# Optimization experiments

Measured on AMD Instinct MI355X. Metric: run time of the kernel, lower is better.

The kernel has to match this reference:

```python
import jax, jax.numpy as jnp
import numpy as np

N = 50000        # graph_size / n_nodes
E = 1250000      # n_edges
NFEAT = 128
NHID = 64
NCLASS = 47
NLAYERS = 4
DT = 1.0
ALPHA = 1.0


def setup_inputs() -> dict:
    key = jax.random.key(0)
    ks = jax.random.split(key, 12)
    stdv = 1.0 / np.sqrt(NHID)  # reset_params uses uniform(-1/sqrt(nhid), 1/sqrt(nhid))
    u = lambda k, shp: jax.random.uniform(k, shp, jnp.float32, -stdv, stdv)
    return {
        "x": jax.random.normal(ks[0], (N, NFEAT), jnp.float32),
        "edge_index": jax.random.randint(ks[1], (2, E), 0, N, jnp.int32),
        # Linear weights stored as (in, out); torch computes x @ W.T + b, same math.
        "enc_w": u(ks[2], (NFEAT, NHID)),
        "enc_b": u(ks[3], (NHID,)),
        "conv_w": u(ks[4], (NHID, NHID)),   # GCNConv.lin weight (no bias)
        "conv_b": u(ks[5], (NHID,)),        # GCNConv bias (added after aggregation)
        "res_w": u(ks[6], (NHID, NHID)),
        "res_b": u(ks[7], (NHID,)),
        "dec_w": u(ks[8], (NHID, NCLASS)),
        "dec_b": u(ks[9], (NCLASS,)),
        # original inits epsilons to zeros; small noise makes the gate nontrivial
        "epsilons": 0.01 * jax.random.normal(ks[10], (NLAYERS, NHID), jnp.float32),
    }


def reference(x, edge_index, enc_w, enc_b, conv_w, conv_b, res_w, res_b,
              dec_w, dec_b, epsilons):
    n = x.shape[0]
    loop = jnp.arange(n, dtype=edge_index.dtype)
    row = jnp.concatenate([edge_index[0], loop])  # add self-loops (PyG default)
    col = jnp.concatenate([edge_index[1], loop])
    deg = jax.ops.segment_sum(jnp.ones_like(row, x.dtype), col, num_segments=n)
    dinv = jnp.where(deg > 0, jax.lax.rsqrt(deg), 0.0)
    norm = dinv[row] * dinv[col]  # D^{-1/2} (A+I) D^{-1/2}

    # eval mode: dropout is identity
    X = jax.nn.relu(x @ enc_w + enc_b)
    X0 = X
    for i in range(NLAYERS):
        h = X @ conv_w  # conv.lin(X), shared by conv and residual v1
        conv_out = jax.ops.segment_sum(h[row] * norm[:, None], col,
                                       num_segments=n) + conv_b
        res = -(h @ res_w + res_b)          # res_connection_v1
        coeff = 1.0 + jnp.tanh(epsilons[i])[None, :]  # (1, nhid) broadcast over nodes
        X0 = X0 * coeff + DT * (jax.nn.relu(conv_out + res) - ALPHA * X)
        X = X0
    return X @ dec_w + dec_b
```

## Files before the change

### kernel.cpp

```cpp
#include <hip/hip_runtime.h>
#include <hip/hip_bf16.h>
#include <math.h>

#define NFEAT 128
#define NHID 64
#define NCLASS 47
#define NLAYERS 4
#define CAP 80
#define NBUCK 8
#define BSHIFT 13
#define BCAP 262144
#define BK_EPB 4096
#define FILL2_KB 64
#define AFW 72

typedef __attribute__((ext_vector_type(8))) _Float16 half8;
typedef __attribute__((ext_vector_type(4))) float f32x4;


__global__ __launch_bounds__(256) void k_init(int* __restrict__ deg,
                                              int* __restrict__ gcur,
                                              const float* __restrict__ conv_w,
                                              const float* __restrict__ res_w,
                                              const float* __restrict__ conv_b,
                                              const float* __restrict__ res_b,
                                              const float* __restrict__ eps,
                                              const float* __restrict__ dec_w,
                                              _Float16* __restrict__ Whb,
                                              _Float16* __restrict__ W2hb,
                                              _Float16* __restrict__ Dechb,
                                              float* __restrict__ bc,
                                              float* __restrict__ te,
                                              int n, int nzero) {
    int gid = blockIdx.x * 256 + threadIdx.x;
    if (gid < nzero) {
        if (gid < n) deg[gid] = 0;
        return;
    }
    int t = gid - nzero;
    if (t < 512) {
        int jt = t >> 7, kt = (t >> 6) & 1, l = t & 63;
        int j = jt * 16 + (l & 15);
        int kb = kt * 32 + (l >> 4) * 8;
#pragma unroll
        for (int i = 0; i < 8; ++i)
            Whb[t * 8 + i] = (_Float16)conv_w[(kb + i) * 64 + j];
        return;
    }
    t -= 512;
    if (t < 512) {
        int jt = t >> 7, kt = (t >> 6) & 1, l = t & 63;
        int j = jt * 16 + (l & 15);
        int kb = kt * 32 + (l >> 4) * 8;
#pragma unroll
        for (int i = 0; i < 8; ++i) {
            int k = kb + i;
            float acc = 0.0f;
#pragma unroll 8
            for (int o = 0; o < 64; ++o)
                acc = fmaf(conv_w[k * 64 + o], res_w[o * 64 + j], acc);
            W2hb[t * 8 + i] = (_Float16)acc;
        }
        return;
    }
    t -= 512;
    if (t < 512) {
        int jt = t >> 7, kt = (t >> 6) & 1, l = t & 63;
        int j = jt * 16 + (l & 15);
        int kb = kt * 32 + (l >> 4) * 8;
#pragma unroll
        for (int i = 0; i < 8; ++i) {
            int k = kb + i;
            Dechb[t * 8 + i] = (j < NCLASS) ? (_Float16)dec_w[k * NCLASS + j]
                                            : (_Float16)0.0f;
        }
        return;
    }
    t -= 512;
    if (t < NLAYERS * NHID) {
        te[t] = tanhf(eps[t]);
        if (t < NHID) bc[t] = conv_b[t] - res_b[t];
        if (t < NBUCK) gcur[t] = 0;
    }
}


__global__ __launch_bounds__(256) void k_bucket(const int* __restrict__ row,
                                                const int* __restrict__ col,
                                                int* __restrict__ gcur,
                                                unsigned int* __restrict__ buckets,
                                                int e) {
    __shared__ int lc[BK_EPB];
    __shared__ int lr[BK_EPB];
    __shared__ int cnt[NBUCK], basep[NBUCK], cnt2[NBUCK];
    const int tid = threadIdx.x;
    const int start = blockIdx.x * BK_EPB;
    const int m = min(BK_EPB, e - start);
    if (tid < NBUCK) { cnt[tid] = 0; cnt2[tid] = 0; }
    __syncthreads();
    for (int i = tid; i < m; i += 256) {
        int c = col[start + i];
        int r = row[start + i];
        lc[i] = c; lr[i] = r;
        atomicAdd(&cnt[c >> BSHIFT], 1);
    }
    __syncthreads();
    if (tid < NBUCK) basep[tid] = atomicAdd(&gcur[tid], cnt[tid]);
    __syncthreads();
    for (int i = tid; i < m; i += 256) {
        int c = lc[i], r = lr[i];
        int s = c >> BSHIFT;
        int dst = basep[s] + atomicAdd(&cnt2[s], 1);
        if (dst < BCAP)
            buckets[(size_t)s * BCAP + dst] = ((unsigned)r << 16) | (unsigned)c;
    }
}


__global__ __launch_bounds__(256) void k_fill2(const unsigned int* __restrict__ buckets,
                                               const int* __restrict__ gcur,
                                               int* __restrict__ deg,
                                               unsigned short* __restrict__ csr) {
    const int s = blockIdx.x & (NBUCK - 1);
    const int k = blockIdx.x >> 3;
    const int cnt = min(gcur[s], BCAP);
    const int per = (cnt + FILL2_KB - 1) / FILL2_KB;
    const int lo = k * per;
    const int hi = min(lo + per, cnt);
    const unsigned int* bp = buckets + (size_t)s * BCAP;
    for (int i = lo + (int)threadIdx.x; i < hi; i += 256) {
        unsigned int v = bp[i];
        int c = (int)(v & 0xffffu);
        int r = (int)(v >> 16);
        int pos = atomicAdd(&deg[c], 1);
        if (pos < CAP) csr[(size_t)c * CAP + pos] = (unsigned short)r;
    }
}


__global__ void k_dinv(const int* __restrict__ deg, float* __restrict__ dinv,
                       float* __restrict__ rsq, unsigned short* __restrict__ csr,
                       _Float16* __restrict__ Y0, _Float16* __restrict__ Y1, int n) {
    int i = blockIdx.x * blockDim.x + threadIdx.x;
    if (i < n) {
        int d = deg[i];
        if (d > CAP) d = CAP;
        float d1 = (float)(deg[i] + 1);
        dinv[i] = rsqrtf(d1);
        rsq[i] = sqrtf(d1);
        int end = (d + 7) & ~7;
        if (end > CAP) end = CAP;
        for (int s = d; s < end; ++s)
            csr[(size_t)i * CAP + s] = (unsigned short)n;
    }
    if (i < NHID) {
        Y0[(size_t)n * NHID + i] = (_Float16)0.0f;
        Y1[(size_t)n * NHID + i] = (_Float16)0.0f;
    }
}


__global__ __launch_bounds__(256) void k_encoder(const float* __restrict__ x,
                                                 const float* __restrict__ w,
                                                 const float* __restrict__ b,
                                                 const float* __restrict__ dinv,
                                                 _Float16* __restrict__ Y, int n) {
    __shared__ float xs[16][NFEAT];
    const int wid = threadIdx.x >> 6;
    const int j = threadIdx.x & 63;
    const int base = blockIdx.x * 16 + wid * 4;
    for (int m = 0; m < 4; ++m) {
        int node = base + m;
        float a = 0.f, c = 0.f;
        if (node < n) {
            a = x[node * NFEAT + j];
            c = x[node * NFEAT + 64 + j];
        }
        xs[wid * 4 + m][j] = a;
        xs[wid * 4 + m][j + 64] = c;
    }
    float acc[4] = {0.f, 0.f, 0.f, 0.f};
#pragma unroll 4
    for (int k4 = 0; k4 < NFEAT / 4; ++k4) {
        int k = k4 * 4;
        float w0 = w[(k + 0) * 64 + j];
        float w1 = w[(k + 1) * 64 + j];
        float w2 = w[(k + 2) * 64 + j];
        float w3 = w[(k + 3) * 64 + j];
        for (int m = 0; m < 4; ++m) {
            const float4 xv = *reinterpret_cast<const float4*>(&xs[wid * 4 + m][k]);
            acc[m] = fmaf(xv.x, w0, fmaf(xv.y, w1, fmaf(xv.z, w2, fmaf(xv.w, w3, acc[m]))));
        }
    }
    float bj = b[j];
    for (int m = 0; m < 4; ++m) {
        int node = base + m;
        if (node < n) {
            float v = fmaxf(acc[m] + bj, 0.0f);
            Y[node * NHID + j] = (_Float16)(v * dinv[node]);
        }
    }
}


__global__ __launch_bounds__(256, 4) void k_layer(
    const half8* __restrict__ Y8c, _Float16* __restrict__ Ynext,
    const int* __restrict__ deg, const unsigned short* __restrict__ csr,
    const float* __restrict__ dinv, const float* __restrict__ rsq,
    const half8* __restrict__ Whb, const half8* __restrict__ W2hb,
    const half8* __restrict__ Dechb,
    const float* __restrict__ bc, const float* __restrict__ te,
    const float* __restrict__ dec_b, float* __restrict__ out, int n, int last) {
    __shared__ _Float16 Af[16][AFW];
    __shared__ _Float16 Xf[16][AFW];
    const int wid = threadIdx.x >> 6;
    const int lane = threadIdx.x & 63;
    const int g = lane >> 4;
    const int l = lane & 15;
    const int c = l & 7;
    const unsigned sh = (l & 8) << 1;
    const int base = blockIdx.x * 16 + wid * 4;
    const int mynode = base + g;
    const bool gact = mynode < n;
    const int gn = gact ? mynode : 0;
    const int rown = gact ? mynode : n;
    const float dcg = dinv[gn];
    const float rcg = rsq[gn];
    int d = gact ? deg[gn] : 0;
    if (d > CAP) d = CAP;
    const int nit = (d + 7) >> 3;

    float acc[8] = {0.f, 0.f, 0.f, 0.f, 0.f, 0.f, 0.f, 0.f};
    const uint4* cp = reinterpret_cast<const uint4*>(csr + (size_t)gn * CAP);

    uint4 rA = cp[0];
    int a0 = (int)((rA.x >> sh) & 0xffffu);
    int a1 = (int)((rA.y >> sh) & 0xffffu);
    int a2 = (int)((rA.z >> sh) & 0xffffu);
    int a3 = (int)((rA.w >> sh) & 0xffffu);
    half8 A0 = Y8c[(size_t)(a0 * 8 + c)];
    half8 A1 = Y8c[(size_t)(a1 * 8 + c)];
    half8 A2 = Y8c[(size_t)(a2 * 8 + c)];
    half8 A3 = Y8c[(size_t)(a3 * 8 + c)];
    int it = 0;
    for (; it + 1 < nit; it += 2) {
        uint4 rB = cp[it + 1];
        int b0 = (int)((rB.x >> sh) & 0xffffu);
        int b1 = (int)((rB.y >> sh) & 0xffffu);
        int b2 = (int)((rB.z >> sh) & 0xffffu);
        int b3 = (int)((rB.w >> sh) & 0xffffu);
        half8 B0 = Y8c[(size_t)(b0 * 8 + c)];
        half8 B1 = Y8c[(size_t)(b1 * 8 + c)];
        half8 B2 = Y8c[(size_t)(b2 * 8 + c)];
        half8 B3 = Y8c[(size_t)(b3 * 8 + c)];
#pragma unroll
        for (int i = 0; i < 8; ++i)
            acc[i] += ((float)A0[i] + (float)A1[i]) + ((float)A2[i] + (float)A3[i]);
        rA = cp[it + 2];
        a0 = (int)((rA.x >> sh) & 0xffffu);
        a1 = (int)((rA.y >> sh) & 0xffffu);
        a2 = (int)((rA.z >> sh) & 0xffffu);
        a3 = (int)((rA.w >> sh) & 0xffffu);
        A0 = Y8c[(size_t)(a0 * 8 + c)];
        A1 = Y8c[(size_t)(a1 * 8 + c)];
        A2 = Y8c[(size_t)(a2 * 8 + c)];
        A3 = Y8c[(size_t)(a3 * 8 + c)];
#pragma unroll
        for (int i = 0; i < 8; ++i)
            acc[i] += ((float)B0[i] + (float)B1[i]) + ((float)B2[i] + (float)B3[i]);
    }
    if (it < nit) {
#pragma unroll
        for (int i = 0; i < 8; ++i)
            acc[i] += ((float)A0[i] + (float)A1[i]) + ((float)A2[i] + (float)A3[i]);
    }
#pragma unroll
    for (int i = 0; i < 8; ++i) acc[i] += __shfl_xor(acc[i], 8);

    if (l < 8) {
        half8 yc = Y8c[(size_t)(rown * 8 + c)];
        half8 hg, hx;
#pragma unroll
        for (int i = 0; i < 8; ++i) {
            float ycf = (float)yc[i];
            hg[i] = (_Float16)((acc[i] + ycf) * dcg);
            hx[i] = (_Float16)(ycf * rcg);
        }
        *reinterpret_cast<half8*>(&Af[wid * 4 + g][c * 8]) = hg;
        *reinterpret_cast<half8*>(&Xf[wid * 4 + g][c * 8]) = hx;
    }

    float dv[4];
#pragma unroll
    for (int i = 0; i < 4; ++i) dv[i] = __shfl(dcg, i * 16);

    const int ar = (wid * 4 + (lane & 15)) & 15;
    const int aq = (lane >> 4) * 8;
    half8 aG0 = *reinterpret_cast<const half8*>(&Af[ar][aq]);
    half8 aG1 = *reinterpret_cast<const half8*>(&Af[ar][32 + aq]);
    half8 aX0 = *reinterpret_cast<const half8*>(&Xf[ar][aq]);
    half8 aX1 = *reinterpret_cast<const half8*>(&Xf[ar][32 + aq]);
    const f32x4 zero = {0.f, 0.f, 0.f, 0.f};

#pragma unroll
    for (int jt = 0; jt < 4; ++jt) {
        half8 bG0 = Whb[(jt * 2 + 0) * 64 + lane];
        half8 bG1 = Whb[(jt * 2 + 1) * 64 + lane];
        half8 bX0 = W2hb[(jt * 2 + 0) * 64 + lane];
        half8 bX1 = W2hb[(jt * 2 + 1) * 64 + lane];
        f32x4 dG = __builtin_amdgcn_mfma_f32_16x16x32_f16(aG0, bG0, zero, 0, 0, 0);
        dG = __builtin_amdgcn_mfma_f32_16x16x32_f16(aG1, bG1, dG, 0, 0, 0);
        f32x4 dX = __builtin_amdgcn_mfma_f32_16x16x32_f16(aX0, bX0, zero, 0, 0, 0);
        dX = __builtin_amdgcn_mfma_f32_16x16x32_f16(aX1, bX1, dX, 0, 0, 0);
        if (lane < 16) {
            int j = jt * 16 + lane;
            float tej = te[j], bcj = bc[j];
#pragma unroll
            for (int i = 0; i < 4; ++i) {
                int node = base + i;
                float xf = (float)Xf[wid * 4 + i][j];
                float xn = xf * tej + fmaxf(dG[i] + bcj - dX[i], 0.0f);
                if (!last) {
                    if (node < n)
                        Ynext[(size_t)node * NHID + j] = (_Float16)(xn * dv[i]);
                } else {
                    Af[wid * 4 + i][j] = (_Float16)xn;
                }
            }
        }
    }

    if (last) {
        half8 aD0 = *reinterpret_cast<const half8*>(&Af[ar][aq]);
        half8 aD1 = *reinterpret_cast<const half8*>(&Af[ar][32 + aq]);
#pragma unroll
        for (int jt = 0; jt < 4; ++jt) {
            half8 bD0 = Dechb[(jt * 2 + 0) * 64 + lane];
            half8 bD1 = Dechb[(jt * 2 + 1) * 64 + lane];
            f32x4 dd = __builtin_amdgcn_mfma_f32_16x16x32_f16(aD0, bD0, zero, 0, 0, 0);
            dd = __builtin_amdgcn_mfma_f32_16x16x32_f16(aD1, bD1, dd, 0, 0, 0);
            if (lane < 16) {
                int j = jt * 16 + lane;
                if (j < NCLASS) {
                    float db = dec_b[j];
#pragma unroll
                    for (int i = 0; i < 4; ++i) {
                        int node = base + i;
                        if (node < n) out[(size_t)node * NCLASS + j] = dd[i] + db;
                    }
                }
            }
        }
    }
}

extern "C" void kernel_launch(void* const* d_in, const int* in_sizes, int n_in,
                              void* d_out, int out_size, void* d_ws, size_t ws_size,
                              hipStream_t stream) {
    const float* x      = (const float*)d_in[0];
    const int*   edges  = (const int*)d_in[1];
    const float* enc_w  = (const float*)d_in[2];
    const float* enc_b  = (const float*)d_in[3];
    const float* conv_w = (const float*)d_in[4];
    const float* conv_b = (const float*)d_in[5];
    const float* res_w  = (const float*)d_in[6];
    const float* res_b  = (const float*)d_in[7];
    const float* dec_w  = (const float*)d_in[8];
    const float* dec_b  = (const float*)d_in[9];
    const float* eps    = (const float*)d_in[10];
    float* out = (float*)d_out;

    const int n = in_sizes[0] / NFEAT;
    const int e = in_sizes[1] / 2;
    const int* row = edges;
    const int* col = edges + e;

    char* p = (char*)d_ws;
    unsigned short* csr = (unsigned short*)p;
    p += ((size_t)n * CAP * 2 + 64 + 15) & ~(size_t)15;
    unsigned int* buckets = (unsigned int*)p;  p += (size_t)NBUCK * BCAP * 4;
    _Float16* Y0 = (_Float16*)p;  p += (((size_t)(n + 1) * NHID * 2 + 15) & ~(size_t)15);
    _Float16* Y1 = (_Float16*)p;  p += (((size_t)(n + 1) * NHID * 2 + 15) & ~(size_t)15);
    int*   deg  = (int*)p;    p += (size_t)n * 4;
    float* dinv = (float*)p;  p += (size_t)n * 4;
    float* rsq  = (float*)p;  p += (size_t)n * 4;
    int*   gcur = (int*)p;    p += 64;
    float* bc   = (float*)p;  p += NHID * 4;
    float* te   = (float*)p;  p += NLAYERS * NHID * 4;
    _Float16* Whb   = (_Float16*)p;  p += 4096 * 2;
    _Float16* W2hb  = (_Float16*)p;  p += 4096 * 2;
    _Float16* Dechb = (_Float16*)p;  p += 4096 * 2;
    if ((size_t)(p - (char*)d_ws) > ws_size) return;

    const int nzero = ((n + 255) / 256) * 256;
    const int init_blocks = (nzero + 1792 + 255) / 256;

    k_init<<<init_blocks, 256, 0, stream>>>(deg, gcur, conv_w, res_w, conv_b, res_b,
                                            eps, dec_w, Whb, W2hb, Dechb, bc, te,
                                            n, nzero);
    const int bblocks = (e + BK_EPB - 1) / BK_EPB;
    k_bucket<<<bblocks, 256, 0, stream>>>(row, col, gcur, buckets, e);
    k_fill2<<<NBUCK * FILL2_KB, 256, 0, stream>>>(buckets, gcur, deg, csr);
    k_dinv<<<(n + 255) / 256, 256, 0, stream>>>(deg, dinv, rsq, csr, Y0, Y1, n);

    const int tblocks = (n + 15) / 16;
    k_encoder<<<tblocks, 256, 0, stream>>>(x, enc_w, enc_b, dinv, Y0, n);

    for (int l = 0; l < NLAYERS; ++l) {
        _Float16* ycur = (l & 1) ? Y1 : Y0;
        _Float16* ynxt = (l & 1) ? Y0 : Y1;
        k_layer<<<tblocks, 256, 0, stream>>>((const half8*)ycur, ynxt, deg, csr,
                                             dinv, rsq, (const half8*)Whb,
                                             (const half8*)W2hb, (const half8*)Dechb,
                                             bc, te + l * NHID, dec_b, out, n,
                                             (l == NLAYERS - 1) ? 1 : 0);
    }
}
```

Before: 257.6 us.

## Use fine-grained node buckets with shared-memory degree counters in CSR fill

Edges are now bucketed into 128 slices of 512 destination nodes instead of 8 large buckets. Each CSR-fill block owns one slice, counts degrees with shared-memory atomics, then writes the degree array once. This removes the global atomics on the degree array and the separate degree-zeroing pass in the init kernel. In exchange the fill kernel runs only one block per slice, which may leave the GPU under-occupied. Correctness also depends on no bucket exceeding the smaller per-bucket capacity.

```diff
diff --git a/kernel.cpp b/kernel.cpp
--- a/kernel.cpp
+++ b/kernel.cpp
@@ -7,19 +7,18 @@
 #define NCLASS 47
 #define NLAYERS 4
 #define CAP 80
-#define NBUCK 8
-#define BSHIFT 13
-#define BCAP 262144
+#define NBUCK 128
+#define BSHIFT 9
+#define BSLICE 512
+#define BCAP 16384
 #define BK_EPB 4096
-#define FILL2_KB 64
 #define AFW 72
 
 typedef __attribute__((ext_vector_type(8))) _Float16 half8;
 typedef __attribute__((ext_vector_type(4))) float f32x4;
 
 
-__global__ __launch_bounds__(256) void k_init(int* __restrict__ deg,
-                                              int* __restrict__ gcur,
+__global__ __launch_bounds__(256) void k_init(int* __restrict__ gcur,
                                               const float* __restrict__ conv_w,
                                               const float* __restrict__ res_w,
                                               const float* __restrict__ conv_b,
@@ -30,14 +29,8 @@
                                               _Float16* __restrict__ W2hb,
                                               _Float16* __restrict__ Dechb,
                                               float* __restrict__ bc,
-                                              float* __restrict__ te,
-                                              int n, int nzero) {
-    int gid = blockIdx.x * 256 + threadIdx.x;
-    if (gid < nzero) {
-        if (gid < n) deg[gid] = 0;
-        return;
-    }
-    int t = gid - nzero;
+                                              float* __restrict__ te) {
+    int t = blockIdx.x * 256 + threadIdx.x;
     if (t < 512) {
         int jt = t >> 7, kt = (t >> 6) & 1, l = t & 63;
         int j = jt * 16 + (l & 15);
@@ -96,7 +89,7 @@
     const int tid = threadIdx.x;
     const int start = blockIdx.x * BK_EPB;
     const int m = min(BK_EPB, e - start);
-    if (tid < NBUCK) { cnt[tid] = 0; cnt2[tid] = 0; }
+    for (int i = tid; i < NBUCK; i += 256) { cnt[i] = 0; cnt2[i] = 0; }
     __syncthreads();
     for (int i = tid; i < m; i += 256) {
         int c = col[start + i];
@@ -105,7 +98,8 @@
         atomicAdd(&cnt[c >> BSHIFT], 1);
     }
     __syncthreads();
-    if (tid < NBUCK) basep[tid] = atomicAdd(&gcur[tid], cnt[tid]);
+    for (int i = tid; i < NBUCK; i += 256)
+        if (cnt[i] > 0) basep[i] = atomicAdd(&gcur[i], cnt[i]);
     __syncthreads();
     for (int i = tid; i < m; i += 256) {
         int c = lc[i], r = lr[i];
@@ -120,21 +114,26 @@
 __global__ __launch_bounds__(256) void k_fill2(const unsigned int* __restrict__ buckets,
                                                const int* __restrict__ gcur,
                                                int* __restrict__ deg,
-                                               unsigned short* __restrict__ csr) {
-    const int s = blockIdx.x & (NBUCK - 1);
-    const int k = blockIdx.x >> 3;
+                                               unsigned short* __restrict__ csr,
+                                               int n) {
+    __shared__ int cur[BSLICE];
+    const int s = blockIdx.x;
+    const int tid = threadIdx.x;
+    for (int i = tid; i < BSLICE; i += 256) cur[i] = 0;
+    __syncthreads();
     const int cnt = min(gcur[s], BCAP);
-    const int per = (cnt + FILL2_KB - 1) / FILL2_KB;
-    const int lo = k * per;
-    const int hi = min(lo + per, cnt);
     const unsigned int* bp = buckets + (size_t)s * BCAP;
-    for (int i = lo + (int)threadIdx.x; i < hi; i += 256) {
+    for (int i = tid; i < cnt; i += 256) {
         unsigned int v = bp[i];
         int c = (int)(v & 0xffffu);
         int r = (int)(v >> 16);
-        int pos = atomicAdd(&deg[c], 1);
+        int pos = atomicAdd(&cur[c & (BSLICE - 1)], 1);
         if (pos < CAP) csr[(size_t)c * CAP + pos] = (unsigned short)r;
     }
+    __syncthreads();
+    const int base = s * BSLICE;
+    const int nb = min(BSLICE, n - base);
+    for (int i = tid; i < nb; i += 256) deg[base + i] = cur[i];
 }
 
 
@@ -384,7 +383,7 @@
     int*   deg  = (int*)p;    p += (size_t)n * 4;
     float* dinv = (float*)p;  p += (size_t)n * 4;
     float* rsq  = (float*)p;  p += (size_t)n * 4;
-    int*   gcur = (int*)p;    p += 64;
+    int*   gcur = (int*)p;    p += ((NBUCK + 15) & ~15) * 4;
     float* bc   = (float*)p;  p += NHID * 4;
     float* te   = (float*)p;  p += NLAYERS * NHID * 4;
     _Float16* Whb   = (_Float16*)p;  p += 4096 * 2;
@@ -392,15 +391,11 @@
     _Float16* Dechb = (_Float16*)p;  p += 4096 * 2;
     if ((size_t)(p - (char*)d_ws) > ws_size) return;
 
-    const int nzero = ((n + 255) / 256) * 256;
-    const int init_blocks = (nzero + 1792 + 255) / 256;
-
-    k_init<<<init_blocks, 256, 0, stream>>>(deg, gcur, conv_w, res_w, conv_b, res_b,
-                                            eps, dec_w, Whb, W2hb, Dechb, bc, te,
-                                            n, nzero);
+    k_init<<<7, 256, 0, stream>>>(gcur, conv_w, res_w, conv_b, res_b,
+                                  eps, dec_w, Whb, W2hb, Dechb, bc, te);
     const int bblocks = (e + BK_EPB - 1) / BK_EPB;
     k_bucket<<<bblocks, 256, 0, stream>>>(row, col, gcur, buckets, e);
-    k_fill2<<<NBUCK * FILL2_KB, 256, 0, stream>>>(buckets, gcur, deg, csr);
+    k_fill2<<<NBUCK, 256, 0, stream>>>(buckets, gcur, deg, csr, n);
     k_dinv<<<(n + 255) / 256, 256, 0, stream>>>(deg, dinv, rsq, csr, Y0, Y1, n);
 
     const int tblocks = (n + 15) / 16;
```

Result: faster. 229.8 us (-10.8%).
